# Optimization experiments

Hardware: AMD Instinct MI355X
Metric: run time of the kernel (lower is better)

Reference implementation:

```python
import jax, jax.numpy as jnp
import numpy as np

CONF_TH = 0.9
FRACTION = 0.66
IGNORE = 255
LAMBDA = 1.0


def _image_mask(max_prob, lab, num_classes):
    """max_prob: [N] float, lab: [N] int32 pseudo labels. Returns [N] bool mask.

    Faithful to the torch loop: per class c, keep the top int(count_c * FRACTION)
    pixels of that class by confidence, OR any pixel with confidence > CONF_TH.
    Implemented with ONE sort per image + within-class cumulative rank.
    """
    N = max_prob.shape[0]
    mask_prob = max_prob > CONF_TH
    # per-class pixel counts and top-k budget (int() truncates in torch)
    counts = jnp.zeros((num_classes,), jnp.int32).at[lab].add(1)
    k = (counts.astype(jnp.float32) * FRACTION).astype(jnp.int32)
    # sort pixels by confidence descending (stable; no ties with random floats)
    order = jnp.argsort(-max_prob)
    lab_s = lab[order]
    # within-class rank in sorted order: rank 0 = most confident pixel of its class
    onehot = jax.nn.one_hot(lab_s, num_classes, dtype=jnp.int32)  # [N, C]
    rank = jnp.take_along_axis(jnp.cumsum(onehot, axis=0), lab_s[:, None], axis=1)[:, 0] - 1
    sel_s = rank < k[lab_s]
    mask_topk = jnp.zeros((N,), bool).at[order].set(sel_s)
    return mask_prob | mask_topk


def setup_inputs() -> dict:
    key = jax.random.key(0)
    pred = jax.random.normal(key, (8, 19, 512, 1024), dtype=jnp.float32)
    return {"pred": pred}


def reference(pred):
    B, C, H, W = pred.shape
    N = H * W
    # teacher is None -> pseudo labels from pred itself (detached)
    pred_sg = jax.lax.stop_gradient(pred)
    prob = jax.nn.softmax(pred_sg, axis=1)
    max_prob = prob.max(axis=1).reshape(B, N)          # [B, N]
    lab = jnp.argmax(pred_sg, axis=1).astype(jnp.int32).reshape(B, N)  # [B, N]
    mask = jax.vmap(lambda mp, l: _image_mask(mp, l, C))(max_prob, lab)  # [B, N] bool
    pseudo = jnp.where(mask, lab, IGNORE)
    # cross-entropy with ignore_index, mean over kept pixels
    logp = jax.nn.log_softmax(pred, axis=1)            # [B, C, H, W]
    logp = logp.transpose(0, 2, 3, 1).reshape(B, N, C)  # [B, N, C]
    valid = pseudo != IGNORE
    tgt = jnp.where(valid, pseudo, 0)
    nll = -jnp.take_along_axis(logp, tgt[:, :, None], axis=2)[:, :, 0]  # [B, N]
    denom = jnp.maximum(jnp.sum(valid), 1).astype(pred.dtype)
    loss = jnp.sum(nll * valid.astype(pred.dtype)) / denom
    return loss * LAMBDA
```

## Files before the change

### kernel.cpp

```cpp
#include <hip/hip_runtime.h>
#include <stdint.h>

#define BLK 256

constexpr int Bsz = 8, Ccls = 19, Hh = 512, Ww = 1024;
constexpr int Npix = Hh * Ww;
constexpr int TotPix = Bsz * Npix;
constexpr int NGroup = Bsz * Ccls;
constexpr int SUBS = 64;
constexpr int NB1 = 256;
constexpr int NB2 = 4096;
constexpr int KEY_BASE = 122 << 5;

__device__ __forceinline__ int key1_of(uint32_t u) {
  int k = (int)(u >> 18) - KEY_BASE;
  return k < 0 ? 0 : (k > 255 ? 255 : k);
}

__global__ __launch_bounds__(BLK) void k_fused(const float* __restrict__ pred,
                                               float4* __restrict__ mp_out,
                                               uchar4* __restrict__ lab_out,
                                               uint32_t* __restrict__ h1g) {
  __shared__ uint32_t hist[Ccls * NB1];
  int t = threadIdx.x;
#pragma unroll
  for (int c = 0; c < Ccls; ++c) hist[c * NB1 + t] = 0;
  __syncthreads();

  int blk = blockIdx.x;
  int b = blk >> 6;
  int s = blk & 63;
  const float* ibase = pred + (size_t)b * Ccls * Npix;
  int n0 = s * 8192;

  for (int j = 0; j < 8; ++j) {
    int n = n0 + j * 1024 + t * 4;
    float4 v[Ccls];
#pragma unroll
    for (int c = 0; c < Ccls; ++c)
      v[c] = *(const float4*)(ibase + (size_t)c * Npix + n);

    float mp[4]; int lc[4];
#pragma unroll
    for (int q = 0; q < 4; ++q) {
      float m = ((const float*)&v[0])[q]; int l = 0;
#pragma unroll
      for (int c = 1; c < Ccls; ++c) {
        float x = ((const float*)&v[c])[q];
        if (x > m) { m = x; l = c; }
      }
      float sum = 0.f;
#pragma unroll
      for (int c = 0; c < Ccls; ++c) sum += __expf(((const float*)&v[c])[q] - m);
      mp[q] = 1.0f / sum;
      lc[q] = l;
      uint32_t u = __float_as_uint(mp[q]);
      atomicAdd(&hist[l * NB1 + key1_of(u)], 1u);
    }
    int p4 = b * (Npix / 4) + n / 4;
    mp_out[p4] = make_float4(mp[0], mp[1], mp[2], mp[3]);
    lab_out[p4] = make_uchar4((uint8_t)lc[0], (uint8_t)lc[1], (uint8_t)lc[2], (uint8_t)lc[3]);
  }

  __syncthreads();
  uint32_t* dst = h1g + (size_t)b * (Ccls * NB1);
#pragma unroll
  for (int c = 0; c < Ccls; ++c) {
    uint32_t v = hist[c * NB1 + t];
    if (v) atomicAdd(&dst[c * NB1 + t], v);
  }
}

__global__ __launch_bounds__(BLK) void k_select1(const uint32_t* __restrict__ h1g,
                                                 int* __restrict__ selhi,
                                                 int* __restrict__ rem) {
  int g = blockIdx.x;
  int b = g / Ccls, c = g % Ccls;
  int t = threadIdx.x;
  int bin = NB1 - 1 - t;
  uint32_t cnt = h1g[(size_t)b * (Ccls * NB1) + c * NB1 + bin];
  __shared__ uint32_t sc[BLK];
  sc[t] = cnt;
  __syncthreads();
  for (int ofs = 1; ofs < BLK; ofs <<= 1) {
    uint32_t vv = (t >= ofs) ? sc[t - ofs] : 0u;
    __syncthreads();
    sc[t] += vv;
    __syncthreads();
  }
  uint32_t incl = sc[t];
  uint32_t excl = incl - cnt;
  uint32_t total = sc[BLK - 1];
  int k = (int)((float)total * 0.66f);
  if (t == 0 && k == 0) { selhi[g] = -1; rem[g] = 0; }
  if (k > 0 && (int)excl < k && k <= (int)incl) {
    selhi[g] = bin;
    rem[g] = k - (int)excl;
  }
}

__global__ __launch_bounds__(BLK) void k_hist2(const float4* __restrict__ mp,
                                               const uchar4* __restrict__ lab,
                                               const int* __restrict__ selhi,
                                               uint32_t* __restrict__ hist2) {
  int p4 = blockIdx.x * BLK + threadIdx.x;
  int b = p4 >> 17;
  float4 m = mp[p4];
  uchar4 l = lab[p4];
  const float* mf = (const float*)&m;
  const uint8_t* lf = (const uint8_t*)&l;
#pragma unroll
  for (int q = 0; q < 4; ++q) {
    uint32_t u = __float_as_uint(mf[q]);
    int g = b * Ccls + (int)lf[q];
    if (key1_of(u) == selhi[g])
      atomicAdd(&hist2[g * NB2 + (int)((u >> 6) & 0xFFFu)], 1u);
  }
}

__global__ __launch_bounds__(BLK) void k_select2(const uint32_t* __restrict__ hist2,
                                                 const int* __restrict__ selhi,
                                                 const int* __restrict__ rem,
                                                 uint32_t* __restrict__ thresh) {
  int g = blockIdx.x;
  int t = threadIdx.x;
  int sh = selhi[g];
  if (sh < 0) { if (t == 0) thresh[g] = 0x7F800000u; return; }
  const uint32_t* h = hist2 + g * NB2;
  uint32_t loc[16]; uint32_t psum = 0;
  int hi = NB2 - 1 - t * 16;
#pragma unroll
  for (int i = 0; i < 16; ++i) { loc[i] = h[hi - i]; psum += loc[i]; }
  __shared__ uint32_t sc[BLK];
  sc[t] = psum;
  __syncthreads();
  for (int ofs = 1; ofs < BLK; ofs <<= 1) {
    uint32_t vv = (t >= ofs) ? sc[t - ofs] : 0u;
    __syncthreads();
    sc[t] += vv;
    __syncthreads();
  }
  uint32_t incl = sc[t];
  int k = rem[g];
  uint32_t excl = incl - psum;
  if (k > 0 && (int)excl < k && k <= (int)incl) {
    uint32_t cum = excl;
#pragma unroll
    for (int i = 0; i < 16; ++i) {
      if ((uint32_t)k <= cum + loc[i]) {
        thresh[g] = ((uint32_t)(sh + KEY_BASE) << 18) | ((uint32_t)(hi - i) << 6);
        break;
      }
      cum += loc[i];
    }
  }
}

__global__ __launch_bounds__(BLK) void k_loss(const float4* __restrict__ mp_arr,
                                              const uchar4* __restrict__ lab,
                                              const uint32_t* __restrict__ thresh,
                                              float* __restrict__ gsum,
                                              uint32_t* __restrict__ gcnt,
                                              uint32_t* __restrict__ gdone,
                                              float* __restrict__ out) {
  int p4 = blockIdx.x * BLK + threadIdx.x;
  int b = p4 >> 17;
  float4 m = mp_arr[p4];
  uchar4 l = lab[p4];
  const float* mf = (const float*)&m;
  const uint8_t* lf = (const uint8_t*)&l;
  float vs = 0.f; uint32_t vc = 0u;
#pragma unroll
  for (int q = 0; q < 4; ++q) {
    float mp = mf[q];
    int g = b * Ccls + (int)lf[q];
    uint32_t u = __float_as_uint(mp);
    bool sel = (mp > 0.9f) || (u >= thresh[g]);
    if (sel) { vs += -logf(mp); vc += 1u; }
  }
#pragma unroll
  for (int o = 32; o > 0; o >>= 1) {
    vs += __shfl_down(vs, o, 64);
    vc += __shfl_down(vc, o, 64);
  }
  __shared__ float ssum[BLK / 64];
  __shared__ uint32_t scnt[BLK / 64];
  int wave = threadIdx.x >> 6;
  int lane = threadIdx.x & 63;
  if (lane == 0) { ssum[wave] = vs; scnt[wave] = vc; }
  __syncthreads();
  if (threadIdx.x == 0) {
    float ts = 0.f; uint32_t tc = 0u;
#pragma unroll
    for (int w = 0; w < BLK / 64; ++w) { ts += ssum[w]; tc += scnt[w]; }
    atomicAdd(gsum, ts);
    atomicAdd(gcnt, tc);
    __threadfence();
    uint32_t ticket = atomicAdd(gdone, 1u);
    if (ticket == gridDim.x - 1) {
      float    sv = atomicAdd(gsum, 0.0f);
      uint32_t cv = atomicAdd(gcnt, 0u);
      out[0] = sv / (float)(cv > 0u ? cv : 1u);
    }
  }
}

extern "C" void kernel_launch(void* const* d_in, const int* in_sizes, int n_in,
                              void* d_out, int out_size, void* d_ws, size_t ws_size,
                              hipStream_t stream) {
  const float* pred = (const float*)d_in[0];
  char* ws = (char*)d_ws;
  size_t off = 0;
  auto carve = [&](size_t bytes) -> void* {
    void* p = ws + off;
    off = (off + bytes + 255) & ~(size_t)255;
    return p;
  };
  float*    mp    = (float*)carve((size_t)TotPix * 4);
  uint8_t*  lab   = (uint8_t*)carve((size_t)TotPix);
  int*      selhi = (int*)carve((size_t)NGroup * 4);
  int*      rem   = (int*)carve((size_t)NGroup * 4);
  uint32_t* thr   = (uint32_t*)carve((size_t)NGroup * 4);
  size_t zero_off = off;
  uint32_t* h1g   = (uint32_t*)carve((size_t)Bsz * Ccls * NB1 * 4);
  uint32_t* hist2 = (uint32_t*)carve((size_t)NGroup * NB2 * 4);
  float*    gsum  = (float*)carve(4);
  uint32_t* gcnt  = (uint32_t*)carve(4);
  uint32_t* gdone = (uint32_t*)carve(4);

  hipMemsetAsync(ws + zero_off, 0, off - zero_off, stream);

  int nblk4 = TotPix / (BLK * 4);
  k_fused  <<<Bsz * SUBS, BLK, 0, stream>>>(pred, (float4*)mp, (uchar4*)lab, h1g);
  k_select1<<<NGroup,     BLK, 0, stream>>>(h1g, selhi, rem);
  k_hist2  <<<nblk4,      BLK, 0, stream>>>((const float4*)mp, (const uchar4*)lab, selhi, hist2);
  k_select2<<<NGroup,     BLK, 0, stream>>>(hist2, selhi, rem, thr);
  k_loss   <<<nblk4,      BLK, 0, stream>>>((const float4*)mp, (const uchar4*)lab, thr,
                                            gsum, gcnt, gdone, (float*)d_out);
}
```

Baseline: 524.8 us.

## Pack label into low mantissa bits and use per-block partial histograms

Stores the 5-bit class label in the low mantissa bits of the max-probability word, so the separate label array is dropped and later passes read a single uint4 per four pixels. The first-level histogram is now written per block to a private slice, replacing global atomics, and select1 sums the 64 slices itself. Truncating the low mantissa bits slightly perturbs the probability values and thresholds; the mp>0.9 and bin-key comparisons can change at bin edges, and the loss uses the truncated value. It also removes some memset work for h1.

```diff
diff --git a/kernel.cpp b/kernel.cpp
--- a/kernel.cpp
+++ b/kernel.cpp
@@ -11,6 +11,7 @@
 constexpr int NB1 = 256;
 constexpr int NB2 = 4096;
 constexpr int KEY_BASE = 122 << 5;
+constexpr uint32_t LABM = 31u;
 
 __device__ __forceinline__ int key1_of(uint32_t u) {
   int k = (int)(u >> 18) - KEY_BASE;
@@ -18,9 +19,8 @@
 }
 
 __global__ __launch_bounds__(BLK) void k_fused(const float* __restrict__ pred,
-                                               float4* __restrict__ mp_out,
-                                               uchar4* __restrict__ lab_out,
-                                               uint32_t* __restrict__ h1g) {
+                                               uint4* __restrict__ mp_out,
+                                               uint32_t* __restrict__ h1) {
   __shared__ uint32_t hist[Ccls * NB1];
   int t = threadIdx.x;
 #pragma unroll
@@ -40,7 +40,7 @@
     for (int c = 0; c < Ccls; ++c)
       v[c] = *(const float4*)(ibase + (size_t)c * Npix + n);
 
-    float mp[4]; int lc[4];
+    uint32_t pk[4];
 #pragma unroll
     for (int q = 0; q < 4; ++q) {
       float m = ((const float*)&v[0])[q]; int l = 0;
@@ -52,33 +52,38 @@
       float sum = 0.f;
 #pragma unroll
       for (int c = 0; c < Ccls; ++c) sum += __expf(((const float*)&v[c])[q] - m);
-      mp[q] = 1.0f / sum;
-      lc[q] = l;
-      uint32_t u = __float_as_uint(mp[q]);
+      float mp = 1.0f / sum;
+      uint32_t u = __float_as_uint(mp);
       atomicAdd(&hist[l * NB1 + key1_of(u)], 1u);
+      pk[q] = (u & ~LABM) | (uint32_t)l;
     }
     int p4 = b * (Npix / 4) + n / 4;
-    mp_out[p4] = make_float4(mp[0], mp[1], mp[2], mp[3]);
-    lab_out[p4] = make_uchar4((uint8_t)lc[0], (uint8_t)lc[1], (uint8_t)lc[2], (uint8_t)lc[3]);
-  }
-
-  __syncthreads();
-  uint32_t* dst = h1g + (size_t)b * (Ccls * NB1);
-#pragma unroll
-  for (int c = 0; c < Ccls; ++c) {
-    uint32_t v = hist[c * NB1 + t];
-    if (v) atomicAdd(&dst[c * NB1 + t], v);
-  }
-}
-
-__global__ __launch_bounds__(BLK) void k_select1(const uint32_t* __restrict__ h1g,
+    mp_out[p4] = make_uint4(pk[0], pk[1], pk[2], pk[3]);
+  }
+
+  __syncthreads();
+  uint32_t* dst = h1 + (size_t)blk * (Ccls * NB1);
+#pragma unroll
+  for (int c = 0; c < Ccls; ++c) dst[c * NB1 + t] = hist[c * NB1 + t];
+}
+
+__global__ __launch_bounds__(BLK) void k_select1(const uint32_t* __restrict__ h1,
                                                  int* __restrict__ selhi,
                                                  int* __restrict__ rem) {
   int g = blockIdx.x;
   int b = g / Ccls, c = g % Ccls;
   int t = threadIdx.x;
   int bin = NB1 - 1 - t;
-  uint32_t cnt = h1g[(size_t)b * (Ccls * NB1) + c * NB1 + bin];
+  const size_t gs = (size_t)Ccls * NB1;
+  const uint32_t* hp = h1 + (size_t)(b * SUBS) * gs + c * NB1 + bin;
+  uint32_t a0 = 0, a1 = 0, a2 = 0, a3 = 0;
+  for (int s = 0; s < SUBS; s += 4) {
+    a0 += hp[(size_t)(s + 0) * gs];
+    a1 += hp[(size_t)(s + 1) * gs];
+    a2 += hp[(size_t)(s + 2) * gs];
+    a3 += hp[(size_t)(s + 3) * gs];
+  }
+  uint32_t cnt = a0 + a1 + a2 + a3;
   __shared__ uint32_t sc[BLK];
   sc[t] = cnt;
   __syncthreads();
@@ -99,20 +104,17 @@
   }
 }
 
-__global__ __launch_bounds__(BLK) void k_hist2(const float4* __restrict__ mp,
-                                               const uchar4* __restrict__ lab,
+__global__ __launch_bounds__(BLK) void k_hist2(const uint4* __restrict__ mp,
                                                const int* __restrict__ selhi,
                                                uint32_t* __restrict__ hist2) {
   int p4 = blockIdx.x * BLK + threadIdx.x;
   int b = p4 >> 17;
-  float4 m = mp[p4];
-  uchar4 l = lab[p4];
-  const float* mf = (const float*)&m;
-  const uint8_t* lf = (const uint8_t*)&l;
+  uint4 m = mp[p4];
+  const uint32_t* mu = (const uint32_t*)&m;
 #pragma unroll
   for (int q = 0; q < 4; ++q) {
-    uint32_t u = __float_as_uint(mf[q]);
-    int g = b * Ccls + (int)lf[q];
+    uint32_t u = mu[q];
+    int g = b * Ccls + (int)(u & LABM);
     if (key1_of(u) == selhi[g])
       atomicAdd(&hist2[g * NB2 + (int)((u >> 6) & 0xFFFu)], 1u);
   }
@@ -156,8 +158,7 @@
   }
 }
 
-__global__ __launch_bounds__(BLK) void k_loss(const float4* __restrict__ mp_arr,
-                                              const uchar4* __restrict__ lab,
+__global__ __launch_bounds__(BLK) void k_loss(const uint4* __restrict__ mp_arr,
                                               const uint32_t* __restrict__ thresh,
                                               float* __restrict__ gsum,
                                               uint32_t* __restrict__ gcnt,
@@ -165,17 +166,15 @@
                                               float* __restrict__ out) {
   int p4 = blockIdx.x * BLK + threadIdx.x;
   int b = p4 >> 17;
-  float4 m = mp_arr[p4];
-  uchar4 l = lab[p4];
-  const float* mf = (const float*)&m;
-  const uint8_t* lf = (const uint8_t*)&l;
+  uint4 m = mp_arr[p4];
+  const uint32_t* mu = (const uint32_t*)&m;
   float vs = 0.f; uint32_t vc = 0u;
 #pragma unroll
   for (int q = 0; q < 4; ++q) {
-    float mp = mf[q];
-    int g = b * Ccls + (int)lf[q];
-    uint32_t u = __float_as_uint(mp);
-    bool sel = (mp > 0.9f) || (u >= thresh[g]);
+    uint32_t u = mu[q];
+    int g = b * Ccls + (int)(u & LABM);
+    float mp = __uint_as_float(u & ~LABM);
+    bool sel = (mp > 0.9f) || ((u & ~LABM) >= thresh[g]);
     if (sel) { vs += -logf(mp); vc += 1u; }
   }
 #pragma unroll
@@ -216,13 +215,12 @@
     off = (off + bytes + 255) & ~(size_t)255;
     return p;
   };
-  float*    mp    = (float*)carve((size_t)TotPix * 4);
-  uint8_t*  lab   = (uint8_t*)carve((size_t)TotPix);
+  uint32_t* mp    = (uint32_t*)carve((size_t)TotPix * 4);
+  uint32_t* h1    = (uint32_t*)carve((size_t)Bsz * SUBS * Ccls * NB1 * 4);
   int*      selhi = (int*)carve((size_t)NGroup * 4);
   int*      rem   = (int*)carve((size_t)NGroup * 4);
   uint32_t* thr   = (uint32_t*)carve((size_t)NGroup * 4);
   size_t zero_off = off;
-  uint32_t* h1g   = (uint32_t*)carve((size_t)Bsz * Ccls * NB1 * 4);
   uint32_t* hist2 = (uint32_t*)carve((size_t)NGroup * NB2 * 4);
   float*    gsum  = (float*)carve(4);
   uint32_t* gcnt  = (uint32_t*)carve(4);
@@ -231,10 +229,10 @@
   hipMemsetAsync(ws + zero_off, 0, off - zero_off, stream);
 
   int nblk4 = TotPix / (BLK * 4);
-  k_fused  <<<Bsz * SUBS, BLK, 0, stream>>>(pred, (float4*)mp, (uchar4*)lab, h1g);
-  k_select1<<<NGroup,     BLK, 0, stream>>>(h1g, selhi, rem);
-  k_hist2  <<<nblk4,      BLK, 0, stream>>>((const float4*)mp, (const uchar4*)lab, selhi, hist2);
+  k_fused  <<<Bsz * SUBS, BLK, 0, stream>>>(pred, (uint4*)mp, h1);
+  k_select1<<<NGroup,     BLK, 0, stream>>>(h1, selhi, rem);
+  k_hist2  <<<nblk4,      BLK, 0, stream>>>((const uint4*)mp, selhi, hist2);
   k_select2<<<NGroup,     BLK, 0, stream>>>(hist2, selhi, rem, thr);
-  k_loss   <<<nblk4,      BLK, 0, stream>>>((const float4*)mp, (const uchar4*)lab, thr,
+  k_loss   <<<nblk4,      BLK, 0, stream>>>((const uint4*)mp, thr,
                                             gsum, gcnt, gdone, (float*)d_out);
 }
```

Result: no change. 525.4 us (+0.1%).
